# Kernel tuning notes

Hardware: AMD Instinct MI355X
Metric: run time of the kernel (lower is better)

## Reference

```python
import jax, jax.numpy as jnp
import numpy as np

N_CODEBOOKS = 9

def _l2norm(v):
    # F.normalize(p=2, eps=1e-12) over last dim
    n = jnp.linalg.norm(v, axis=-1, keepdims=True)
    return v / jnp.maximum(n, 1e-12)


def setup_inputs() -> dict:
    key = jax.random.key(0)
    ks = jax.random.split(key, 6)
    B, D, T = 4, 64, 32768
    n, K, cd = N_CODEBOOKS, 1024, 8
    return {
        "x": jax.random.normal(ks[0], (B, D, T), jnp.float32),
        "W_in": jax.random.normal(ks[1], (n, cd, D), jnp.float32) * (1.0 / np.sqrt(D)),
        "b_in": jnp.zeros((n, cd), jnp.float32),
        "codebooks": jax.random.normal(ks[2], (n, K, cd), jnp.float32),
        "W_out": jax.random.normal(ks[3], (n, D, cd), jnp.float32) * (1.0 / np.sqrt(cd)),
        "b_out": jnp.zeros((n, D), jnp.float32),
    }


def _rvq(x, W_in, b_in, codebooks, W_out, b_out):
    # Residual vector quantization (DAC ResidualVectorQuantize.forward), all codebooks used.
    n = W_in.shape[0]
    sg = jax.lax.stop_gradient
    residual = x                       # [B, D, T]
    z_q = jnp.zeros_like(x)
    commit = jnp.float32(0.0)
    cb_loss = jnp.float32(0.0)
    codes, lat = [], []
    for i in range(n):
        # in_proj: 1x1 conv D -> cd
        z_e = jnp.einsum('cd,bdt->bct', W_in[i], residual) + b_in[i][None, :, None]  # [B,cd,T]
        enc = _l2norm(z_e.transpose(0, 2, 1))   # [B,T,cd], L2-normalized
        cbk = _l2norm(codebooks[i])             # [K,cd],  L2-normalized
        # squared euclidean distance between normalized vectors
        dist = (jnp.sum(enc * enc, -1, keepdims=True)
                - 2.0 * jnp.einsum('btc,kc->btk', enc, cbk)
                + jnp.sum(cbk * cbk, -1)[None, None, :])  # [B,T,K]
        idx = jnp.argmin(dist, axis=-1)          # [B,T]
        z_q_i = codebooks[i][idx].transpose(0, 2, 1)  # gather -> [B,cd,T]
        commit = commit + jnp.mean((z_e - sg(z_q_i)) ** 2)
        cb_loss = cb_loss + jnp.mean((z_q_i - sg(z_e)) ** 2)
        # straight-through estimator
        z_st = z_e + sg(z_q_i - z_e)
        # out_proj: 1x1 conv cd -> D
        out_i = jnp.einsum('dc,bct->bdt', W_out[i], z_st) + b_out[i][None, :, None]
        z_q = z_q + out_i
        residual = residual - out_i
        codes.append(idx)
        lat.append(z_e)
    codes = jnp.stack(codes, axis=1)         # [B, n, T]
    latents = jnp.concatenate(lat, axis=1)   # [B, n*cd, T]
    # DACRVQBottleneck divides losses by num_quantizers
    return z_q, codes, latents, commit / n, cb_loss / n


def reference(x, W_in, b_in, codebooks, W_out, b_out):
    return _rvq(x, W_in, b_in, codebooks, W_out, b_out)
```

## Files before the change

kernel.cpp:

```cpp
#include <hip/hip_runtime.h>

#define NCB 9
#define KCB 1024
#define CD 8
#define DD 64
#define TT 32768
#define BB 4

#define ZQ_SZ (BB*DD*TT)
#define CODES_OFF ZQ_SZ
#define CODES_SZ (BB*NCB*TT)
#define LAT_OFF (CODES_OFF + CODES_SZ)
#define LAT_SZ (BB*NCB*CD*TT)
#define LOSS_OFF (LAT_OFF + LAT_SZ)

#define OFF_CBSPLIT  0
#define OFF_CBN64    294912
#define OFF_SCBK64   884736
#define OFF_WIN64    958464
#define OFF_WOUT64   995328
#define OFF_BIN64    1032192
#define OFF_BOUT64   1032768
#define OFF_LOSSPART 1037376

#define MARGIN 1.5e-4f

typedef __attribute__((ext_vector_type(8))) short short8;
typedef __attribute__((ext_vector_type(4))) float f32x4;

__device__ __forceinline__ unsigned bf16rtn(float x) {
  unsigned u = __float_as_uint(x);
  return (u + 0x7fffu + ((u >> 16) & 1u)) >> 16;
}

__global__ void prep_cb(const float* __restrict__ cb,
                        unsigned* __restrict__ cbsplit,
                        double* __restrict__ cbn64, double* __restrict__ scbk64) {
  int r = blockIdx.x * blockDim.x + threadIdx.x;
  if (r >= NCB * KCB) return;
  double v[CD], s = 0.0;
#pragma unroll
  for (int c = 0; c < CD; c++) { v[c] = (double)cb[r*CD + c]; s += v[c]*v[c]; }
  double den = fmax(sqrt(s), 1e-12);
  double s2 = 0.0;
  float of[CD];
#pragma unroll
  for (int c = 0; c < CD; c++) {
    double o = v[c] / den;
    cbn64[r*CD + c] = o;
    of[c] = (float)o;
    s2 += o*o;
  }
  scbk64[r] = s2;
  unsigned hp[4], lp[4];
#pragma unroll
  for (int c2 = 0; c2 < 4; c2++) {
    float f0 = of[2*c2], f1 = of[2*c2+1];
    unsigned h0 = bf16rtn(f0), h1 = bf16rtn(f1);
    float g0 = f0 - __uint_as_float(h0 << 16);
    float g1 = f1 - __uint_as_float(h1 << 16);
    unsigned l0 = bf16rtn(g0), l1 = bf16rtn(g1);
    hp[c2] = h0 | (h1 << 16);
    lp[c2] = l0 | (l1 << 16);
  }
  int4* dst = (int4*)(cbsplit + (size_t)r*8);
  dst[0] = make_int4((int)hp[0], (int)hp[1], (int)hp[2], (int)hp[3]);
  dst[1] = make_int4((int)lp[0], (int)lp[1], (int)lp[2], (int)lp[3]);
}

__global__ void prep_w(const float* __restrict__ W_in, const float* __restrict__ b_in,
                       const float* __restrict__ W_out, const float* __restrict__ b_out,
                       double* __restrict__ Win64, double* __restrict__ bin64,
                       double* __restrict__ Wout64, double* __restrict__ bout64) {
  int i = blockIdx.x * blockDim.x + threadIdx.x;
  if (i < NCB*CD*DD) Win64[i]  = (double)W_in[i];
  if (i < NCB*CD*DD) Wout64[i] = (double)W_out[i];
  if (i < NCB*CD)    bin64[i]  = (double)b_in[i];
  if (i < NCB*DD)    bout64[i] = (double)b_out[i];
}

#define MERGE(bA,b2A,iA, bB,b2B,iB) { \
  float nb2_ = fmaxf(fminf((bA),(bB)), fmaxf((b2A),(b2B))); \
  bool tk_ = ((bB) > (bA)) || ((bB) == (bA) && (iB) < (iA)); \
  (bA) = fmaxf((bA),(bB)); (b2A) = nb2_; (iA) = tk_ ? (iB) : (iA); }

#define QSEL(Cv, bq, s2, kb, kbv) { \
  float m_ = fmaxf(fmaxf(fmaxf((Cv)[0],(Cv)[1]),(Cv)[2]),(Cv)[3]); \
  float ob_ = (bq); \
  (s2) = __builtin_amdgcn_fmed3f(ob_, (s2), m_); \
  (bq) = fmaxf(ob_, m_); \
  (kb) = (m_ > ob_) ? (kbv) : (kb); }

__global__ __launch_bounds__(512, 2) void rvq_kernel(
    const float* __restrict__ x,
    const float* __restrict__ cb,
    const double* __restrict__ Win64,
    const double* __restrict__ bin64,
    const double* __restrict__ Wout64,
    const double* __restrict__ bout64,
    const unsigned* __restrict__ cbsplit,
    const double* __restrict__ cbn64,
    const double* __restrict__ scbk64,
    float* __restrict__ out,
    double* __restrict__ loss_part) {
  __shared__ __align__(16) char ldsbuf[32768 + 16384];
  __shared__ double wsum[8];

  const int lane = threadIdx.x & 63;
  const int wv   = threadIdx.x >> 6;
  const int tid  = blockIdx.x * 512 + threadIdx.x;
  const int b = tid >> 15;
  const int t = tid & (TT - 1);
  const int lanebase = (lane >> 4) * 4;
  char* bex = ldsbuf + 32768 + wv * 2048;

  double r[DD];
#pragma unroll
  for (int d = 0; d < DD; d++) r[d] = (double)x[(b*DD + d)*TT + t];

  double lacc = 0.0;

  const int stid = (int)threadIdx.x ^ (((int)threadIdx.x >> 3) & 3);
  const int ac0 = 2*(lane & 15) + ((lane >> 4) >> 1);
  const char* abase = ldsbuf + (size_t)(ac0 ^ ((ac0 >> 3) & 3)) * 16;

#pragma unroll 1
  for (int i = 0; i < NCB; i++) {
    __syncthreads();
    {
      const float4* __restrict__ src = (const float4*)(cbsplit + (size_t)i*KCB*8);
      float4* __restrict__ dst = (float4*)ldsbuf;
#pragma unroll
      for (int c0 = 0; c0 < 4; c0++)
        dst[c0*512 + stid] = src[c0*512 + threadIdx.x];
    }
    __syncthreads();

    double ze[CD];
#pragma unroll
    for (int c = 0; c < CD; c++) ze[c] = bin64[i*CD + c];
#pragma unroll
    for (int c = 0; c < CD; c++) {
#pragma unroll
      for (int d = 0; d < DD; d++)
        ze[c] = fma(Win64[(i*CD + c)*DD + d], r[d], ze[c]);
    }

    double s0 = 0.0;
#pragma unroll
    for (int c = 0; c < CD; c++) s0 = fma(ze[c], ze[c], s0);
    double inv = 1.0 / fmax(sqrt(s0), 1e-12);
    float encf[CD];
#pragma unroll
    for (int c = 0; c < CD; c++) encf[c] = (float)(ze[c] * inv);

#pragma unroll
    for (int c = 0; c < CD; c++)
      out[LAT_OFF + (b*NCB*CD + i*CD + c)*TT + t] = (float)ze[c];

    {
      unsigned hp[4], lp[4];
#pragma unroll
      for (int c2 = 0; c2 < 4; c2++) {
        float f0 = encf[2*c2], f1 = encf[2*c2+1];
        unsigned h0 = bf16rtn(f0), h1 = bf16rtn(f1);
        float g0 = f0 - __uint_as_float(h0 << 16);
        float g1 = f1 - __uint_as_float(h1 << 16);
        unsigned l0 = bf16rtn(g0), l1 = bf16rtn(g1);
        hp[c2] = h0 | (h1 << 16);
        lp[c2] = l0 | (l1 << 16);
      }
      *(int4*)(bex + lane*32)      = make_int4((int)hp[0],(int)hp[1],(int)hp[2],(int)hp[3]);
      *(int4*)(bex + lane*32 + 16) = make_int4((int)lp[0],(int)lp[1],(int)lp[2],(int)lp[3]);
    }

    short8 bf0, bf1, bf2, bf3;
    {
      const int boff = (lane & 15)*32 + ((lane >> 4) & 1)*16;
      bf0 = __builtin_bit_cast(short8, *(const int4*)(bex + boff));
      bf1 = __builtin_bit_cast(short8, *(const int4*)(bex + 512 + boff));
      bf2 = __builtin_bit_cast(short8, *(const int4*)(bex + 1024 + boff));
      bf3 = __builtin_bit_cast(short8, *(const int4*)(bex + 1536 + boff));
    }

    float bq0=-3.4e38f, bq1=-3.4e38f, bq2=-3.4e38f, bq3=-3.4e38f;
    float s20=-3.4e38f, s21=-3.4e38f, s22=-3.4e38f, s23=-3.4e38f;
    int kb0=0, kb1=0, kb2=0, kb3=0;
    const f32x4 zero = {0.f, 0.f, 0.f, 0.f};
    int4 a_next = *(const int4*)(abase);
#pragma unroll 4
    for (int ct = 0; ct < 64; ct++) {
      int4 a_cur = a_next;
      if (ct < 63) a_next = *(const int4*)(abase + (ct + 1)*512);
      short8 af8 = __builtin_bit_cast(short8, a_cur);
      const int kbv = ct*16 + lanebase;
      f32x4 C0 = __builtin_amdgcn_mfma_f32_16x16x32_bf16(af8, bf0, zero, 0, 0, 0);
      QSEL(C0, bq0, s20, kb0, kbv);
      f32x4 C1 = __builtin_amdgcn_mfma_f32_16x16x32_bf16(af8, bf1, zero, 0, 0, 0);
      QSEL(C1, bq1, s21, kb1, kbv);
      f32x4 C2 = __builtin_amdgcn_mfma_f32_16x16x32_bf16(af8, bf2, zero, 0, 0, 0);
      QSEL(C2, bq2, s22, kb2, kbv);
      f32x4 C3 = __builtin_amdgcn_mfma_f32_16x16x32_bf16(af8, bf3, zero, 0, 0, 0);
      QSEL(C3, bq3, s23, kb3, kbv);
    }

#pragma unroll
    for (int m = 16; m <= 32; m <<= 1) {
      float ob0 = __shfl_xor(bq0, m, 64), o20 = __shfl_xor(s20, m, 64); int oi0 = __shfl_xor(kb0, m, 64);
      MERGE(bq0, s20, kb0, ob0, o20, oi0);
      float ob1 = __shfl_xor(bq1, m, 64), o21 = __shfl_xor(s21, m, 64); int oi1 = __shfl_xor(kb1, m, 64);
      MERGE(bq1, s21, kb1, ob1, o21, oi1);
      float ob2 = __shfl_xor(bq2, m, 64), o22 = __shfl_xor(s22, m, 64); int oi2 = __shfl_xor(kb2, m, 64);
      MERGE(bq2, s22, kb2, ob2, o22, oi2);
      float ob3 = __shfl_xor(bq3, m, 64), o23 = __shfl_xor(s23, m, 64); int oi3 = __shfl_xor(kb3, m, 64);
      MERGE(bq3, s23, kb3, ob3, o23, oi3);
    }
    const int myp = lane >> 4;
    float b2F = (myp == 0) ? s20 : (myp == 1) ? s21 : (myp == 2) ? s22 : s23;
    int   kbF = (myp == 0) ? kb0 : (myp == 1) ? kb1 : (myp == 2) ? kb2 : kb3;

    float rbest = -3.402823466e38f, rsec = -3.402823466e38f;
    int bidxF = kbF;
#pragma unroll
    for (int j = 0; j < 3 + 1; j++) {
      int k = kbF + j;
      int ch = (2*k) ^ (((2*k) >> 3) & 3);
      int cl = (2*k + 1) ^ (((2*k + 1) >> 3) & 3);
      int4 hv = *(const int4*)(ldsbuf + (size_t)ch*16);
      int4 lv = *(const int4*)(ldsbuf + (size_t)cl*16);
      float dot = 0.f;
      {
        float e;
        e = __uint_as_float(((unsigned)hv.x) << 16) + __uint_as_float(((unsigned)lv.x) << 16);
        dot = fmaf(encf[0], e, dot);
        e = __uint_as_float(((unsigned)hv.x) & 0xFFFF0000u) + __uint_as_float(((unsigned)lv.x) & 0xFFFF0000u);
        dot = fmaf(encf[1], e, dot);
        e = __uint_as_float(((unsigned)hv.y) << 16) + __uint_as_float(((unsigned)lv.y) << 16);
        dot = fmaf(encf[2], e, dot);
        e = __uint_as_float(((unsigned)hv.y) & 0xFFFF0000u) + __uint_as_float(((unsigned)lv.y) & 0xFFFF0000u);
        dot = fmaf(encf[3], e, dot);
        e = __uint_as_float(((unsigned)hv.z) << 16) + __uint_as_float(((unsigned)lv.z) << 16);
        dot = fmaf(encf[4], e, dot);
        e = __uint_as_float(((unsigned)hv.z) & 0xFFFF0000u) + __uint_as_float(((unsigned)lv.z) & 0xFFFF0000u);
        dot = fmaf(encf[5], e, dot);
        e = __uint_as_float(((unsigned)hv.w) << 16) + __uint_as_float(((unsigned)lv.w) << 16);
        dot = fmaf(encf[6], e, dot);
        e = __uint_as_float(((unsigned)hv.w) & 0xFFFF0000u) + __uint_as_float(((unsigned)lv.w) & 0xFFFF0000u);
        dot = fmaf(encf[7], e, dot);
      }
      if (dot > rbest) { rsec = rbest; rbest = dot; bidxF = k; }
      else             { rsec = fmaxf(rsec, dot); }
    }
    bool trigF = (rbest - fmaxf(b2F, rsec)) < MARGIN;

    {
      unsigned long long bal = __ballot(trigF);
      while (bal) {
        int j = __builtin_ctzll(bal);
        bal &= bal - 1;
        double invb = __shfl(inv, j, 64);
        double encb[CD], se = 0.0;
#pragma unroll
        for (int c = 0; c < CD; c++) {
          encb[c] = __shfl(ze[c], j, 64) * invb;
          se = fma(encb[c], encb[c], se);
        }
        const double* __restrict__ cbr = cbn64 + (size_t)i*KCB*CD;
        const double* __restrict__ s64 = scbk64 + i*KCB;
        double bd = 1e300;
        int bk = 0;
#pragma unroll 2
        for (int it = 0; it < 16; it++) {
          int k = it*64 + lane;
          const double* row = cbr + (size_t)k*CD;
          double dot = 0.0;
#pragma unroll
          for (int c = 0; c < CD; c++) dot = fma(encb[c], row[c], dot);
          double dist = fma(-2.0, dot, se) + s64[k];
          if (dist < bd) { bd = dist; bk = k; }
        }
#pragma unroll
        for (int m = 1; m <= 32; m <<= 1) {
          double od = __shfl_xor(bd, m, 64);
          int    ok = __shfl_xor(bk, m, 64);
          bool take = (od < bd) || (od == bd && ok < bk);
          bd = take ? od : bd;
          bk = take ? ok : bk;
        }
        if (lane == j) bidxF = bk;
      }
    }

    const float4* __restrict__ qrow = (const float4*)(cb + (size_t)(i*KCB + bidxF)*CD);
    float4 q0 = qrow[0], q1 = qrow[1];
    double zq[CD] = {(double)q0.x, (double)q0.y, (double)q0.z, (double)q0.w,
                     (double)q1.x, (double)q1.y, (double)q1.z, (double)q1.w};

#pragma unroll
    for (int c = 0; c < CD; c++) {
      double dlt = ze[c] - zq[c];
      lacc = fma(dlt, dlt, lacc);
    }

#pragma unroll
    for (int d = 0; d < DD; d++) {
      double acc = bout64[i*DD + d];
#pragma unroll
      for (int c = 0; c < CD; c++)
        acc = fma(Wout64[(i*DD + d)*CD + c], zq[c], acc);
      r[d] -= acc;
    }

    out[CODES_OFF + (b*NCB + i)*TT + t] = (float)bidxF;
  }

#pragma unroll
  for (int d = 0; d < DD; d++)
    out[(b*DD + d)*TT + t] = (float)((double)x[(b*DD + d)*TT + t] - r[d]);

#pragma unroll
  for (int off = 32; off > 0; off >>= 1)
    lacc += __shfl_down(lacc, off, 64);
  if ((threadIdx.x & 63) == 0) wsum[wv] = lacc;
  __syncthreads();
  if (threadIdx.x == 0) {
    double s = 0.0;
#pragma unroll
    for (int w = 0; w < 8; w++) s += wsum[w];
    loss_part[blockIdx.x] = s;
  }
}

__global__ void loss_final(const double* __restrict__ loss_part,
                           float* __restrict__ out) {
  __shared__ double sh[256];
  sh[threadIdx.x] = loss_part[threadIdx.x];
  __syncthreads();
  for (int off = 128; off > 0; off >>= 1) {
    if (threadIdx.x < off) sh[threadIdx.x] += sh[threadIdx.x + off];
    __syncthreads();
  }
  if (threadIdx.x == 0) {
    double v = sh[0] / ((double)NCB * (double)BB * (double)CD * (double)TT);
    out[LOSS_OFF]     = (float)v;
    out[LOSS_OFF + 1] = (float)v;
  }
}

extern "C" void kernel_launch(void* const* d_in, const int* in_sizes, int n_in,
                              void* d_out, int out_size, void* d_ws, size_t ws_size,
                              hipStream_t stream) {
  const float* x     = (const float*)d_in[0];
  const float* W_in  = (const float*)d_in[1];
  const float* b_in  = (const float*)d_in[2];
  const float* cb    = (const float*)d_in[3];
  const float* W_out = (const float*)d_in[4];
  const float* b_out = (const float*)d_in[5];
  float* out = (float*)d_out;

  char* ws = (char*)d_ws;
  unsigned* cbsplit = (unsigned*)(ws + OFF_CBSPLIT);
  double* cbn64  = (double*)(ws + OFF_CBN64);
  double* scbk64 = (double*)(ws + OFF_SCBK64);
  double* Win64  = (double*)(ws + OFF_WIN64);
  double* Wout64 = (double*)(ws + OFF_WOUT64);
  double* bin64  = (double*)(ws + OFF_BIN64);
  double* bout64 = (double*)(ws + OFF_BOUT64);
  double* loss_part = (double*)(ws + OFF_LOSSPART);

  prep_cb<<<(NCB*KCB + 255)/256, 256, 0, stream>>>(cb, cbsplit, cbn64, scbk64);
  prep_w<<<(NCB*CD*DD + 255)/256, 256, 0, stream>>>(W_in, b_in, W_out, b_out,
                                                    Win64, bin64, Wout64, bout64);
  rvq_kernel<<<256, 512, 0, stream>>>(x, cb, Win64, bin64, Wout64, bout64,
                                      cbsplit, cbn64, scbk64, out, loss_part);
  loss_final<<<1, 256, 0, stream>>>(loss_part, out);
}
```

Baseline: 417.2 us.

## Split codebook search across two waves per token group to double grid parallelism

Each group of 64 tokens is now handled by two waves, and each wave scans half of the codebook tiles with MFMA. The two partial top-2 results are merged through shared memory after a block barrier. The grid doubles to 512 blocks, and only one half writes the outputs and loss. This is meant to fill more CUs on the GPU and shorten the per-wave argmin loop. In exchange, both waves redo the fp64 in/out projections and residual update, and each codebook iteration gets an extra barrier.

```diff
diff --git a/kernel.cpp b/kernel.cpp
--- a/kernel.cpp
+++ b/kernel.cpp
@@ -104,13 +104,17 @@
     float* __restrict__ out,
     double* __restrict__ loss_part) {
   __shared__ __align__(16) char ldsbuf[32768 + 16384];
+  __shared__ float mb[512], m2[512];
+  __shared__ int   mi[512];
   __shared__ double wsum[8];
 
   const int lane = threadIdx.x & 63;
   const int wv   = threadIdx.x >> 6;
-  const int tid  = blockIdx.x * 512 + threadIdx.x;
-  const int b = tid >> 15;
-  const int t = tid & (TT - 1);
+  const int grp  = wv >> 1;
+  const int half = wv & 1;
+  const int p    = blockIdx.x * 256 + grp * 64 + lane;
+  const int b = p >> 15;
+  const int t = p & (TT - 1);
   const int lanebase = (lane >> 4) * 4;
   char* bex = ldsbuf + 32768 + wv * 2048;
 
@@ -154,9 +158,11 @@
 #pragma unroll
     for (int c = 0; c < CD; c++) encf[c] = (float)(ze[c] * inv);
 
-#pragma unroll
-    for (int c = 0; c < CD; c++)
-      out[LAT_OFF + (b*NCB*CD + i*CD + c)*TT + t] = (float)ze[c];
+    if (half == 0) {
+#pragma unroll
+      for (int c = 0; c < CD; c++)
+        out[LAT_OFF + (b*NCB*CD + i*CD + c)*TT + t] = (float)ze[c];
+    }
 
     {
       unsigned hp[4], lp[4];
@@ -187,11 +193,13 @@
     float s20=-3.4e38f, s21=-3.4e38f, s22=-3.4e38f, s23=-3.4e38f;
     int kb0=0, kb1=0, kb2=0, kb3=0;
     const f32x4 zero = {0.f, 0.f, 0.f, 0.f};
-    int4 a_next = *(const int4*)(abase);
+    const int ct0 = half * 32;
+    int4 a_next = *(const int4*)(abase + ct0*512);
 #pragma unroll 4
-    for (int ct = 0; ct < 64; ct++) {
+    for (int cc = 0; cc < 32; cc++) {
+      const int ct = ct0 + cc;
       int4 a_cur = a_next;
-      if (ct < 63) a_next = *(const int4*)(abase + (ct + 1)*512);
+      if (cc < 31) a_next = *(const int4*)(abase + (ct + 1)*512);
       short8 af8 = __builtin_bit_cast(short8, a_cur);
       const int kbv = ct*16 + lanebase;
       f32x4 C0 = __builtin_amdgcn_mfma_f32_16x16x32_bf16(af8, bf0, zero, 0, 0, 0);
@@ -222,7 +230,7 @@
     float rbest = -3.402823466e38f, rsec = -3.402823466e38f;
     int bidxF = kbF;
 #pragma unroll
-    for (int j = 0; j < 3 + 1; j++) {
+    for (int j = 0; j < 4; j++) {
       int k = kbF + j;
       int ch = (2*k) ^ (((2*k) >> 3) & 3);
       int cl = (2*k + 1) ^ (((2*k + 1) >> 3) & 3);
@@ -251,7 +259,19 @@
       if (dot > rbest) { rsec = rbest; rbest = dot; bidxF = k; }
       else             { rsec = fmaxf(rsec, dot); }
     }
-    bool trigF = (rbest - fmaxf(b2F, rsec)) < MARGIN;
+    float secF = fmaxf(b2F, rsec);
+
+    mb[wv*64 + lane] = rbest;
+    m2[wv*64 + lane] = secF;
+    mi[wv*64 + lane] = bidxF;
+    __syncthreads();
+    {
+      int pw = wv ^ 1;
+      float ob = mb[pw*64 + lane], o2 = m2[pw*64 + lane];
+      int   oi = mi[pw*64 + lane];
+      MERGE(rbest, secF, bidxF, ob, o2, oi);
+    }
+    bool trigF = (rbest - secF < MARGIN);
 
     {
       unsigned long long bal = __ballot(trigF);
@@ -296,10 +316,12 @@
     double zq[CD] = {(double)q0.x, (double)q0.y, (double)q0.z, (double)q0.w,
                      (double)q1.x, (double)q1.y, (double)q1.z, (double)q1.w};
 
-#pragma unroll
-    for (int c = 0; c < CD; c++) {
-      double dlt = ze[c] - zq[c];
-      lacc = fma(dlt, dlt, lacc);
+    if (half == 0) {
+#pragma unroll
+      for (int c = 0; c < CD; c++) {
+        double dlt = ze[c] - zq[c];
+        lacc = fma(dlt, dlt, lacc);
+      }
     }
 
 #pragma unroll
@@ -311,12 +333,14 @@
       r[d] -= acc;
     }
 
-    out[CODES_OFF + (b*NCB + i)*TT + t] = (float)bidxF;
-  }
-
-#pragma unroll
-  for (int d = 0; d < DD; d++)
-    out[(b*DD + d)*TT + t] = (float)((double)x[(b*DD + d)*TT + t] - r[d]);
+    if (half == 0) out[CODES_OFF + (b*NCB + i)*TT + t] = (float)bidxF;
+  }
+
+  if (half == 0) {
+#pragma unroll
+    for (int d = 0; d < DD; d++)
+      out[(b*DD + d)*TT + t] = (float)((double)x[(b*DD + d)*TT + t] - r[d]);
+  }
 
 #pragma unroll
   for (int off = 32; off > 0; off >>= 1)
@@ -334,7 +358,8 @@
 __global__ void loss_final(const double* __restrict__ loss_part,
                            float* __restrict__ out) {
   __shared__ double sh[256];
-  sh[threadIdx.x] = loss_part[threadIdx.x];
+  double s = loss_part[threadIdx.x] + loss_part[threadIdx.x + 256];
+  sh[threadIdx.x] = s;
   __syncthreads();
   for (int off = 128; off > 0; off >>= 1) {
     if (threadIdx.x < off) sh[threadIdx.x] += sh[threadIdx.x + off];
@@ -371,7 +396,7 @@
   prep_cb<<<(NCB*KCB + 255)/256, 256, 0, stream>>>(cb, cbsplit, cbn64, scbk64);
   prep_w<<<(NCB*CD*DD + 255)/256, 256, 0, stream>>>(W_in, b_in, W_out, b_out,
                                                     Win64, bin64, Wout64, bout64);
-  rvq_kernel<<<256, 512, 0, stream>>>(x, cb, Win64, bin64, Wout64, bout64,
+  rvq_kernel<<<512, 512, 0, stream>>>(x, cb, Win64, bin64, Wout64, bout64,
                                       cbsplit, cbn64, scbk64, out, loss_part);
   loss_final<<<1, 256, 0, stream>>>(loss_part, out);
 }
```

Result: slower. 870.7 us (+108.7%).

## Split fused RVQ kernel into per-codebook launches with residual kept in global memory

Applied to the files above, without the earlier changes.

Replaces the single persistent kernel, which holds a 64-double residual per thread in registers across all nine codebooks, with nine per-layer launches of 512 blocks of 256 threads. The residual is stored as fp64 in workspace between layers, which frees registers and allows more concurrent waves. The cost is heavy extra global traffic: the 64 MB fp64 residual is read twice and written once per layer, plus nine launch overheads. The new path runs only when the workspace is large enough, otherwise the old kernel is used.

```diff
diff --git a/kernel.cpp b/kernel.cpp
--- a/kernel.cpp
+++ b/kernel.cpp
@@ -22,6 +22,8 @@
 #define OFF_BIN64    1032192
 #define OFF_BOUT64   1032768
 #define OFF_LOSSPART 1037376
+#define OFF_RESID    1054720
+#define WS_NEED_MP   (OFF_RESID + (size_t)BB*DD*TT*8)
 
 #define MARGIN 1.5e-4f
 
@@ -90,6 +92,252 @@
   (s2) = __builtin_amdgcn_fmed3f(ob_, (s2), m_); \
   (bq) = fmaxf(ob_, m_); \
   (kb) = (m_ > ob_) ? (kbv) : (kb); }
+
+__device__ __forceinline__ int search_body(
+    const char* __restrict__ ldsbuf, char* __restrict__ bex,
+    const float* encf, const double* ze, double inv,
+    const double* __restrict__ cbn64, const double* __restrict__ scbk64,
+    int i, int lane) {
+  const int lanebase = (lane >> 4) * 4;
+  {
+    unsigned hp[4], lp[4];
+#pragma unroll
+    for (int c2 = 0; c2 < 4; c2++) {
+      float f0 = encf[2*c2], f1 = encf[2*c2+1];
+      unsigned h0 = bf16rtn(f0), h1 = bf16rtn(f1);
+      float g0 = f0 - __uint_as_float(h0 << 16);
+      float g1 = f1 - __uint_as_float(h1 << 16);
+      unsigned l0 = bf16rtn(g0), l1 = bf16rtn(g1);
+      hp[c2] = h0 | (h1 << 16);
+      lp[c2] = l0 | (l1 << 16);
+    }
+    *(int4*)(bex + lane*32)      = make_int4((int)hp[0],(int)hp[1],(int)hp[2],(int)hp[3]);
+    *(int4*)(bex + lane*32 + 16) = make_int4((int)lp[0],(int)lp[1],(int)lp[2],(int)lp[3]);
+  }
+  short8 bf0, bf1, bf2, bf3;
+  {
+    const int boff = (lane & 15)*32 + ((lane >> 4) & 1)*16;
+    bf0 = __builtin_bit_cast(short8, *(const int4*)(bex + boff));
+    bf1 = __builtin_bit_cast(short8, *(const int4*)(bex + 512 + boff));
+    bf2 = __builtin_bit_cast(short8, *(const int4*)(bex + 1024 + boff));
+    bf3 = __builtin_bit_cast(short8, *(const int4*)(bex + 1536 + boff));
+  }
+  const int ac0 = 2*(lane & 15) + ((lane >> 4) >> 1);
+  const char* abase = ldsbuf + (size_t)(ac0 ^ ((ac0 >> 3) & 3)) * 16;
+
+  float bq0=-3.4e38f, bq1=-3.4e38f, bq2=-3.4e38f, bq3=-3.4e38f;
+  float s20=-3.4e38f, s21=-3.4e38f, s22=-3.4e38f, s23=-3.4e38f;
+  int kb0=0, kb1=0, kb2=0, kb3=0;
+  const f32x4 zero = {0.f, 0.f, 0.f, 0.f};
+  int4 a_next = *(const int4*)(abase);
+#pragma unroll 4
+  for (int ct = 0; ct < 64; ct++) {
+    int4 a_cur = a_next;
+    if (ct < 63) a_next = *(const int4*)(abase + (ct + 1)*512);
+    short8 af8 = __builtin_bit_cast(short8, a_cur);
+    const int kbv = ct*16 + lanebase;
+    f32x4 C0 = __builtin_amdgcn_mfma_f32_16x16x32_bf16(af8, bf0, zero, 0, 0, 0);
+    QSEL(C0, bq0, s20, kb0, kbv);
+    f32x4 C1 = __builtin_amdgcn_mfma_f32_16x16x32_bf16(af8, bf1, zero, 0, 0, 0);
+    QSEL(C1, bq1, s21, kb1, kbv);
+    f32x4 C2 = __builtin_amdgcn_mfma_f32_16x16x32_bf16(af8, bf2, zero, 0, 0, 0);
+    QSEL(C2, bq2, s22, kb2, kbv);
+    f32x4 C3 = __builtin_amdgcn_mfma_f32_16x16x32_bf16(af8, bf3, zero, 0, 0, 0);
+    QSEL(C3, bq3, s23, kb3, kbv);
+  }
+#pragma unroll
+  for (int m = 16; m <= 32; m <<= 1) {
+    float ob0 = __shfl_xor(bq0, m, 64), o20 = __shfl_xor(s20, m, 64); int oi0 = __shfl_xor(kb0, m, 64);
+    MERGE(bq0, s20, kb0, ob0, o20, oi0);
+    float ob1 = __shfl_xor(bq1, m, 64), o21 = __shfl_xor(s21, m, 64); int oi1 = __shfl_xor(kb1, m, 64);
+    MERGE(bq1, s21, kb1, ob1, o21, oi1);
+    float ob2 = __shfl_xor(bq2, m, 64), o22 = __shfl_xor(s22, m, 64); int oi2 = __shfl_xor(kb2, m, 64);
+    MERGE(bq2, s22, kb2, ob2, o22, oi2);
+    float ob3 = __shfl_xor(bq3, m, 64), o23 = __shfl_xor(s23, m, 64); int oi3 = __shfl_xor(kb3, m, 64);
+    MERGE(bq3, s23, kb3, ob3, o23, oi3);
+  }
+  const int myp = lane >> 4;
+  float b2F = (myp == 0) ? s20 : (myp == 1) ? s21 : (myp == 2) ? s22 : s23;
+  int   kbF = (myp == 0) ? kb0 : (myp == 1) ? kb1 : (myp == 2) ? kb2 : kb3;
+
+  float rbest = -3.402823466e38f, rsec = -3.402823466e38f;
+  int bidxF = kbF;
+#pragma unroll
+  for (int j = 0; j < 4; j++) {
+    int k = kbF + j;
+    int ch = (2*k) ^ (((2*k) >> 3) & 3);
+    int cl = (2*k + 1) ^ (((2*k + 1) >> 3) & 3);
+    int4 hv = *(const int4*)(ldsbuf + (size_t)ch*16);
+    int4 lv = *(const int4*)(ldsbuf + (size_t)cl*16);
+    float dot = 0.f;
+    float e;
+    e = __uint_as_float(((unsigned)hv.x) << 16) + __uint_as_float(((unsigned)lv.x) << 16);
+    dot = fmaf(encf[0], e, dot);
+    e = __uint_as_float(((unsigned)hv.x) & 0xFFFF0000u) + __uint_as_float(((unsigned)lv.x) & 0xFFFF0000u);
+    dot = fmaf(encf[1], e, dot);
+    e = __uint_as_float(((unsigned)hv.y) << 16) + __uint_as_float(((unsigned)lv.y) << 16);
+    dot = fmaf(encf[2], e, dot);
+    e = __uint_as_float(((unsigned)hv.y) & 0xFFFF0000u) + __uint_as_float(((unsigned)lv.y) & 0xFFFF0000u);
+    dot = fmaf(encf[3], e, dot);
+    e = __uint_as_float(((unsigned)hv.z) << 16) + __uint_as_float(((unsigned)lv.z) << 16);
+    dot = fmaf(encf[4], e, dot);
+    e = __uint_as_float(((unsigned)hv.z) & 0xFFFF0000u) + __uint_as_float(((unsigned)lv.z) & 0xFFFF0000u);
+    dot = fmaf(encf[5], e, dot);
+    e = __uint_as_float(((unsigned)hv.w) << 16) + __uint_as_float(((unsigned)lv.w) << 16);
+    dot = fmaf(encf[6], e, dot);
+    e = __uint_as_float(((unsigned)hv.w) & 0xFFFF0000u) + __uint_as_float(((unsigned)lv.w) & 0xFFFF0000u);
+    dot = fmaf(encf[7], e, dot);
+    if (dot > rbest) { rsec = rbest; rbest = dot; bidxF = k; }
+    else             { rsec = fmaxf(rsec, dot); }
+  }
+  bool trigF = (rbest - fmaxf(b2F, rsec)) < MARGIN;
+
+  {
+    unsigned long long bal = __ballot(trigF);
+    while (bal) {
+      int j = __builtin_ctzll(bal);
+      bal &= bal - 1;
+      double invb = __shfl(inv, j, 64);
+      double encb[CD], se = 0.0;
+#pragma unroll
+      for (int c = 0; c < CD; c++) {
+        encb[c] = __shfl(ze[c], j, 64) * invb;
+        se = fma(encb[c], encb[c], se);
+      }
+      const double* __restrict__ cbr = cbn64 + (size_t)i*KCB*CD;
+      const double* __restrict__ s64 = scbk64 + i*KCB;
+      double bd = 1e300;
+      int bk = 0;
+#pragma unroll 2
+      for (int it = 0; it < 16; it++) {
+        int k = it*64 + lane;
+        const double* row = cbr + (size_t)k*CD;
+        double dot = 0.0;
+#pragma unroll
+        for (int c = 0; c < CD; c++) dot = fma(encb[c], row[c], dot);
+        double dist = fma(-2.0, dot, se) + s64[k];
+        if (dist < bd) { bd = dist; bk = k; }
+      }
+#pragma unroll
+      for (int m = 1; m <= 32; m <<= 1) {
+        double od = __shfl_xor(bd, m, 64);
+        int    ok = __shfl_xor(bk, m, 64);
+        bool take = (od < bd) || (od == bd && ok < bk);
+        bd = take ? od : bd;
+        bk = take ? ok : bk;
+      }
+      if (lane == j) bidxF = bk;
+    }
+  }
+  return bidxF;
+}
+
+__global__ __launch_bounds__(256, 2) void rvq_layer(
+    int i, int first, int last,
+    const float* __restrict__ x,
+    const float* __restrict__ cb,
+    const double* __restrict__ Win64,
+    const double* __restrict__ bin64,
+    const double* __restrict__ Wout64,
+    const double* __restrict__ bout64,
+    const unsigned* __restrict__ cbsplit,
+    const double* __restrict__ cbn64,
+    const double* __restrict__ scbk64,
+    double* __restrict__ resid,
+    float* __restrict__ out,
+    double* __restrict__ loss_part) {
+  __shared__ __align__(16) char ldsbuf[32768 + 8192];
+  __shared__ double wsum[4];
+
+  const int lane = threadIdx.x & 63;
+  const int wv   = threadIdx.x >> 6;
+  const int tid  = blockIdx.x * 256 + threadIdx.x;
+  const int b = tid >> 15;
+  const int t = tid & (TT - 1);
+  char* bex = ldsbuf + 32768 + wv * 2048;
+
+  {
+    const float4* __restrict__ src = (const float4*)(cbsplit + (size_t)i*KCB*8);
+    float4* __restrict__ dst = (float4*)ldsbuf;
+    const int stid = (int)threadIdx.x ^ (((int)threadIdx.x >> 3) & 3);
+#pragma unroll
+    for (int c0 = 0; c0 < 8; c0++)
+      dst[c0*256 + stid] = src[c0*256 + threadIdx.x];
+  }
+  __syncthreads();
+
+  double ze[CD];
+#pragma unroll
+  for (int c = 0; c < CD; c++) ze[c] = bin64[i*CD + c];
+  {
+    const double* __restrict__ W = Win64 + i*CD*DD;
+#pragma unroll 8
+    for (int d = 0; d < DD; d++) {
+      double rv = first ? (double)x[(b*DD + d)*TT + t]
+                        : resid[(size_t)(b*DD + d)*TT + t];
+#pragma unroll
+      for (int c = 0; c < CD; c++)
+        ze[c] = fma(W[c*DD + d], rv, ze[c]);
+    }
+  }
+
+  double s0 = 0.0;
+#pragma unroll
+  for (int c = 0; c < CD; c++) s0 = fma(ze[c], ze[c], s0);
+  double inv = 1.0 / fmax(sqrt(s0), 1e-12);
+  float encf[CD];
+#pragma unroll
+  for (int c = 0; c < CD; c++) encf[c] = (float)(ze[c] * inv);
+
+#pragma unroll
+  for (int c = 0; c < CD; c++)
+    out[LAT_OFF + ((size_t)b*NCB*CD + i*CD + c)*TT + t] = (float)ze[c];
+
+  int bidxF = search_body(ldsbuf, bex, encf, ze, inv, cbn64, scbk64, i, lane);
+
+  const float4* __restrict__ qrow = (const float4*)(cb + (size_t)(i*KCB + bidxF)*CD);
+  float4 q0 = qrow[0], q1 = qrow[1];
+  double zq[CD] = {(double)q0.x, (double)q0.y, (double)q0.z, (double)q0.w,
+                   (double)q1.x, (double)q1.y, (double)q1.z, (double)q1.w};
+
+  double lacc = 0.0;
+#pragma unroll
+  for (int c = 0; c < CD; c++) {
+    double dlt = ze[c] - zq[c];
+    lacc = fma(dlt, dlt, lacc);
+  }
+
+  {
+    const double* __restrict__ Wo = Wout64 + (size_t)i*DD*CD;
+#pragma unroll 8
+    for (int d = 0; d < DD; d++) {
+      double acc = bout64[i*DD + d];
+#pragma unroll
+      for (int c = 0; c < CD; c++)
+        acc = fma(Wo[d*CD + c], zq[c], acc);
+      double rv = first ? (double)x[(b*DD + d)*TT + t]
+                        : resid[(size_t)(b*DD + d)*TT + t];
+      double rn = rv - acc;
+      resid[(size_t)(b*DD + d)*TT + t] = rn;
+      if (last)
+        out[((size_t)b*DD + d)*TT + t] =
+            (float)((double)x[(b*DD + d)*TT + t] - rn);
+    }
+  }
+
+  out[CODES_OFF + ((size_t)b*NCB + i)*TT + t] = (float)bidxF;
+
+#pragma unroll
+  for (int off = 32; off > 0; off >>= 1)
+    lacc += __shfl_down(lacc, off, 64);
+  if ((threadIdx.x & 63) == 0) wsum[wv] = lacc;
+  __syncthreads();
+  if (threadIdx.x == 0) {
+    double s = wsum[0] + wsum[1] + wsum[2] + wsum[3];
+    if (first) loss_part[blockIdx.x] = s;
+    else       loss_part[blockIdx.x] += s;
+  }
+}
 
 __global__ __launch_bounds__(512, 2) void rvq_kernel(
     const float* __restrict__ x,
@@ -111,7 +359,6 @@
   const int tid  = blockIdx.x * 512 + threadIdx.x;
   const int b = tid >> 15;
   const int t = tid & (TT - 1);
-  const int lanebase = (lane >> 4) * 4;
   char* bex = ldsbuf + 32768 + wv * 2048;
 
   double r[DD];
@@ -119,10 +366,7 @@
   for (int d = 0; d < DD; d++) r[d] = (double)x[(b*DD + d)*TT + t];
 
   double lacc = 0.0;
-
   const int stid = (int)threadIdx.x ^ (((int)threadIdx.x >> 3) & 3);
-  const int ac0 = 2*(lane & 15) + ((lane >> 4) >> 1);
-  const char* abase = ldsbuf + (size_t)(ac0 ^ ((ac0 >> 3) & 3)) * 16;
 
 #pragma unroll 1
   for (int i = 0; i < NCB; i++) {
@@ -156,140 +400,9 @@
 
 #pragma unroll
     for (int c = 0; c < CD; c++)
-      out[LAT_OFF + (b*NCB*CD + i*CD + c)*TT + t] = (float)ze[c];
-
-    {
-      unsigned hp[4], lp[4];
-#pragma unroll
-      for (int c2 = 0; c2 < 4; c2++) {
-        float f0 = encf[2*c2], f1 = encf[2*c2+1];
-        unsigned h0 = bf16rtn(f0), h1 = bf16rtn(f1);
-        float g0 = f0 - __uint_as_float(h0 << 16);
-        float g1 = f1 - __uint_as_float(h1 << 16);
-        unsigned l0 = bf16rtn(g0), l1 = bf16rtn(g1);
-        hp[c2] = h0 | (h1 << 16);
-        lp[c2] = l0 | (l1 << 16);
-      }
-      *(int4*)(bex + lane*32)      = make_int4((int)hp[0],(int)hp[1],(int)hp[2],(int)hp[3]);
-      *(int4*)(bex + lane*32 + 16) = make_int4((int)lp[0],(int)lp[1],(int)lp[2],(int)lp[3]);
-    }
-
-    short8 bf0, bf1, bf2, bf3;
-    {
-      const int boff = (lane & 15)*32 + ((lane >> 4) & 1)*16;
-      bf0 = __builtin_bit_cast(short8, *(const int4*)(bex + boff));
-      bf1 = __builtin_bit_cast(short8, *(const int4*)(bex + 512 + boff));
-      bf2 = __builtin_bit_cast(short8, *(const int4*)(bex + 1024 + boff));
-      bf3 = __builtin_bit_cast(short8, *(const int4*)(bex + 1536 + boff));
-    }
-
-    float bq0=-3.4e38f, bq1=-3.4e38f, bq2=-3.4e38f, bq3=-3.4e38f;
-    float s20=-3.4e38f, s21=-3.4e38f, s22=-3.4e38f, s23=-3.4e38f;
-    int kb0=0, kb1=0, kb2=0, kb3=0;
-    const f32x4 zero = {0.f, 0.f, 0.f, 0.f};
-    int4 a_next = *(const int4*)(abase);
-#pragma unroll 4
-    for (int ct = 0; ct < 64; ct++) {
-      int4 a_cur = a_next;
-      if (ct < 63) a_next = *(const int4*)(abase + (ct + 1)*512);
-      short8 af8 = __builtin_bit_cast(short8, a_cur);
-      const int kbv = ct*16 + lanebase;
-      f32x4 C0 = __builtin_amdgcn_mfma_f32_16x16x32_bf16(af8, bf0, zero, 0, 0, 0);
-      QSEL(C0, bq0, s20, kb0, kbv);
-      f32x4 C1 = __builtin_amdgcn_mfma_f32_16x16x32_bf16(af8, bf1, zero, 0, 0, 0);
-      QSEL(C1, bq1, s21, kb1, kbv);
-      f32x4 C2 = __builtin_amdgcn_mfma_f32_16x16x32_bf16(af8, bf2, zero, 0, 0, 0);
-      QSEL(C2, bq2, s22, kb2, kbv);
-      f32x4 C3 = __builtin_amdgcn_mfma_f32_16x16x32_bf16(af8, bf3, zero, 0, 0, 0);
-      QSEL(C3, bq3, s23, kb3, kbv);
-    }
-
-#pragma unroll
-    for (int m = 16; m <= 32; m <<= 1) {
-      float ob0 = __shfl_xor(bq0, m, 64), o20 = __shfl_xor(s20, m, 64); int oi0 = __shfl_xor(kb0, m, 64);
-      MERGE(bq0, s20, kb0, ob0, o20, oi0);
-      float ob1 = __shfl_xor(bq1, m, 64), o21 = __shfl_xor(s21, m, 64); int oi1 = __shfl_xor(kb1, m, 64);
-      MERGE(bq1, s21, kb1, ob1, o21, oi1);
-      float ob2 = __shfl_xor(bq2, m, 64), o22 = __shfl_xor(s22, m, 64); int oi2 = __shfl_xor(kb2, m, 64);
-      MERGE(bq2, s22, kb2, ob2, o22, oi2);
-      float ob3 = __shfl_xor(bq3, m, 64), o23 = __shfl_xor(s23, m, 64); int oi3 = __shfl_xor(kb3, m, 64);
-      MERGE(bq3, s23, kb3, ob3, o23, oi3);
-    }
-    const int myp = lane >> 4;
-    float b2F = (myp == 0) ? s20 : (myp == 1) ? s21 : (myp == 2) ? s22 : s23;
-    int   kbF = (myp == 0) ? kb0 : (myp == 1) ? kb1 : (myp == 2) ? kb2 : kb3;
-
-    float rbest = -3.402823466e38f, rsec = -3.402823466e38f;
-    int bidxF = kbF;
-#pragma unroll
-    for (int j = 0; j < 3 + 1; j++) {
-      int k = kbF + j;
-      int ch = (2*k) ^ (((2*k) >> 3) & 3);
-      int cl = (2*k + 1) ^ (((2*k + 1) >> 3) & 3);
-      int4 hv = *(const int4*)(ldsbuf + (size_t)ch*16);
-      int4 lv = *(const int4*)(ldsbuf + (size_t)cl*16);
-      float dot = 0.f;
-      {
-        float e;
-        e = __uint_as_float(((unsigned)hv.x) << 16) + __uint_as_float(((unsigned)lv.x) << 16);
-        dot = fmaf(encf[0], e, dot);
-        e = __uint_as_float(((unsigned)hv.x) & 0xFFFF0000u) + __uint_as_float(((unsigned)lv.x) & 0xFFFF0000u);
-        dot = fmaf(encf[1], e, dot);
-        e = __uint_as_float(((unsigned)hv.y) << 16) + __uint_as_float(((unsigned)lv.y) << 16);
-        dot = fmaf(encf[2], e, dot);
-        e = __uint_as_float(((unsigned)hv.y) & 0xFFFF0000u) + __uint_as_float(((unsigned)lv.y) & 0xFFFF0000u);
-        dot = fmaf(encf[3], e, dot);
-        e = __uint_as_float(((unsigned)hv.z) << 16) + __uint_as_float(((unsigned)lv.z) << 16);
-        dot = fmaf(encf[4], e, dot);
-        e = __uint_as_float(((unsigned)hv.z) & 0xFFFF0000u) + __uint_as_float(((unsigned)lv.z) & 0xFFFF0000u);
-        dot = fmaf(encf[5], e, dot);
-        e = __uint_as_float(((unsigned)hv.w) << 16) + __uint_as_float(((unsigned)lv.w) << 16);
-        dot = fmaf(encf[6], e, dot);
-        e = __uint_as_float(((unsigned)hv.w) & 0xFFFF0000u) + __uint_as_float(((unsigned)lv.w) & 0xFFFF0000u);
-        dot = fmaf(encf[7], e, dot);
-      }
-      if (dot > rbest) { rsec = rbest; rbest = dot; bidxF = k; }
-      else             { rsec = fmaxf(rsec, dot); }
-    }
-    bool trigF = (rbest - fmaxf(b2F, rsec)) < MARGIN;
-
-    {
-      unsigned long long bal = __ballot(trigF);
-      while (bal) {
-        int j = __builtin_ctzll(bal);
-        bal &= bal - 1;
-        double invb = __shfl(inv, j, 64);
-        double encb[CD], se = 0.0;
-#pragma unroll
-        for (int c = 0; c < CD; c++) {
-          encb[c] = __shfl(ze[c], j, 64) * invb;
-          se = fma(encb[c], encb[c], se);
-        }
-        const double* __restrict__ cbr = cbn64 + (size_t)i*KCB*CD;
-        const double* __restrict__ s64 = scbk64 + i*KCB;
-        double bd = 1e300;
-        int bk = 0;
-#pragma unroll 2
-        for (int it = 0; it < 16; it++) {
-          int k = it*64 + lane;
-          const double* row = cbr + (size_t)k*CD;
-          double dot = 0.0;
-#pragma unroll
-          for (int c = 0; c < CD; c++) dot = fma(encb[c], row[c], dot);
-          double dist = fma(-2.0, dot, se) + s64[k];
-          if (dist < bd) { bd = dist; bk = k; }
-        }
-#pragma unroll
-        for (int m = 1; m <= 32; m <<= 1) {
-          double od = __shfl_xor(bd, m, 64);
-          int    ok = __shfl_xor(bk, m, 64);
-          bool take = (od < bd) || (od == bd && ok < bk);
-          bd = take ? od : bd;
-          bk = take ? ok : bk;
-        }
-        if (lane == j) bidxF = bk;
-      }
-    }
+      out[LAT_OFF + ((size_t)b*NCB*CD + i*CD + c)*TT + t] = (float)ze[c];
+
+    int bidxF = search_body(ldsbuf, bex, encf, ze, inv, cbn64, scbk64, i, lane);
 
     const float4* __restrict__ qrow = (const float4*)(cb + (size_t)(i*KCB + bidxF)*CD);
     float4 q0 = qrow[0], q1 = qrow[1];
@@ -311,12 +424,12 @@
       r[d] -= acc;
     }
 
-    out[CODES_OFF + (b*NCB + i)*TT + t] = (float)bidxF;
+    out[CODES_OFF + ((size_t)b*NCB + i)*TT + t] = (float)bidxF;
   }
 
 #pragma unroll
   for (int d = 0; d < DD; d++)
-    out[(b*DD + d)*TT + t] = (float)((double)x[(b*DD + d)*TT + t] - r[d]);
+    out[((size_t)b*DD + d)*TT + t] = (float)((double)x[(b*DD + d)*TT + t] - r[d]);
 
 #pragma unroll
   for (int off = 32; off > 0; off >>= 1)
@@ -332,9 +445,11 @@
 }
 
 __global__ void loss_final(const double* __restrict__ loss_part,
-                           float* __restrict__ out) {
+                           float* __restrict__ out, int n) {
   __shared__ double sh[256];
-  sh[threadIdx.x] = loss_part[threadIdx.x];
+  double s = 0.0;
+  for (int k = threadIdx.x; k < n; k += 256) s += loss_part[k];
+  sh[threadIdx.x] = s;
   __syncthreads();
   for (int off = 128; off > 0; off >>= 1) {
     if (threadIdx.x < off) sh[threadIdx.x] += sh[threadIdx.x + off];
@@ -367,11 +482,21 @@
   double* bin64  = (double*)(ws + OFF_BIN64);
   double* bout64 = (double*)(ws + OFF_BOUT64);
   double* loss_part = (double*)(ws + OFF_LOSSPART);
+  double* resid  = (double*)(ws + OFF_RESID);
 
   prep_cb<<<(NCB*KCB + 255)/256, 256, 0, stream>>>(cb, cbsplit, cbn64, scbk64);
   prep_w<<<(NCB*CD*DD + 255)/256, 256, 0, stream>>>(W_in, b_in, W_out, b_out,
                                                     Win64, bin64, Wout64, bout64);
-  rvq_kernel<<<256, 512, 0, stream>>>(x, cb, Win64, bin64, Wout64, bout64,
-                                      cbsplit, cbn64, scbk64, out, loss_part);
-  loss_final<<<1, 256, 0, stream>>>(loss_part, out);
-}
+  if (ws_size >= WS_NEED_MP) {
+    for (int i = 0; i < NCB; i++)
+      rvq_layer<<<512, 256, 0, stream>>>(i, i == 0, i == NCB - 1,
+                                         x, cb, Win64, bin64, Wout64, bout64,
+                                         cbsplit, cbn64, scbk64, resid, out,
+                                         loss_part);
+    loss_final<<<1, 256, 0, stream>>>(loss_part, out, 512);
+  } else {
+    rvq_kernel<<<256, 512, 0, stream>>>(x, cb, Win64, bin64, Wout64, bout64,
+                                        cbsplit, cbn64, scbk64, out, loss_part);
+    loss_final<<<1, 256, 0, stream>>>(loss_part, out, 256);
+  }
+}
```

After: 641.0 us. 1.54x slower.
